# Kernel optimization log

Measured on AMD Instinct MI355X. Metric: run time of the kernel, lower is better.

Reference implementation:

```python
import jax, jax.numpy as jnp
import numpy as np
import math
from jax import lax

B, M, T = 32, 80, 10000
EPS = 1e-6
DELTA_CLAMP = (0.001, 0.1)


def setup_inputs() -> dict:
    key = jax.random.key(0)
    k_mel, = jax.random.split(key, 1)
    # linear mel energies: non-negative
    mel = jax.random.uniform(k_mel, (B, M, T), dtype=jnp.float32)

    def full(v):
        return jnp.full((M,), v, dtype=jnp.float32)

    # exact init values from the torch module
    log_s = full(math.log(0.15 / (1 - 0.15)))
    log_alpha = full(math.log(0.99 / (1 - 0.99)))
    log_delta = full(math.log(0.01))
    log_r = full(math.log(0.1 / (1 - 0.1)))
    return {"mel": mel, "log_s": log_s, "log_alpha": log_alpha,
            "log_delta": log_delta, "log_r": log_r}


def reference(mel, log_s, log_alpha, log_delta, log_r):
    # per-channel coefficients, clamped exactly as in torch
    s = jnp.clip(jax.nn.sigmoid(log_s), 0.05, 0.3)            # (M,)
    alpha = jnp.clip(jax.nn.sigmoid(log_alpha), 0.9, 0.999)   # (M,)
    delta = jnp.clip(jnp.exp(log_delta), *DELTA_CLAMP)        # (M,)
    r = jnp.clip(jax.nn.sigmoid(log_r), 0.05, 0.25)           # (M,)

    # EMA smoother along time via scan. Torch inits smoother = mel[:,:,0]
    # and the t=0 update yields (1-s)*mel0 + s*mel0 = mel0, so we scan over
    # all T frames with init = mel[:,:,0].
    s_bm = s[None, :]                      # (1, M) broadcasts over (B, M)

    def step(smoother, x_t):
        new = (1.0 - s_bm) * smoother + s_bm * x_t
        return new, new

    xs = jnp.moveaxis(mel, -1, 0)          # (T, B, M)
    _, sm = lax.scan(step, mel[:, :, 0], xs)
    smoothed = jnp.moveaxis(sm, 0, -1)     # (B, M, T)

    alpha_c = alpha[None, :, None]
    delta_c = delta[None, :, None]
    r_c = r[None, :, None]

    gain = (EPS + smoothed) ** (-alpha_c)
    pcen = (mel * gain + delta_c) ** r_c - delta_c ** r_c
    return pcen
```

## Files before the change

kernel.cpp:

```cpp
#include <hip/hip_runtime.h>
#include <math.h>


constexpr int B_ = 32, M_ = 80, T_ = 10000;
constexpr int EPI = 256;
constexpr int NFULL = T_ / EPI;
constexpr float EPS_ = 1e-6f;

__device__ __forceinline__ float pcen_one(float x, float y, float alpha,
                                          float delta, float r, float dr) {
    float g = __expf(-alpha * __logf(y + EPS_));
    float z = fmaf(x, g, delta);
    return __expf(r * __logf(z)) - dr;
}

__global__ __launch_bounds__(256) void pcen_kernel(
    const float* __restrict__ mel,
    const float* __restrict__ log_s,
    const float* __restrict__ log_alpha,
    const float* __restrict__ log_delta,
    const float* __restrict__ log_r,
    float* __restrict__ out)
{
    const int lane = threadIdx.x & 63;
    const int wave = threadIdx.x >> 6;
    const int row  = blockIdx.x * 4 + wave;
    if (row >= B_ * M_) return;
    const int m = row % M_;

    float s = 1.0f / (1.0f + __expf(-log_s[m]));
    s = fminf(fmaxf(s, 0.05f), 0.3f);
    float alpha = 1.0f / (1.0f + __expf(-log_alpha[m]));
    alpha = fminf(fmaxf(alpha, 0.9f), 0.999f);
    float delta = __expf(log_delta[m]);
    delta = fminf(fmaxf(delta, 0.001f), 0.1f);
    float r = 1.0f / (1.0f + __expf(-log_r[m]));
    r = fminf(fmaxf(r, 0.05f), 0.25f);

    const float a  = 1.0f - s;
    const float dr = __expf(r * __logf(delta));
    const float a2 = a * a, a3 = a2 * a, a4 = a2 * a2;
    const float c0 = a4, c1 = c0 * c0, c2 = c1 * c1,
                c3 = c2 * c2, c4 = c3 * c3, c5 = c4 * c4;
    const float a256  = c5 * c5;
    const float a4lane = __expf(__logf(a) * (float)(4 * lane));

    const size_t rb = (size_t)row * T_;
    const float* mp = mel + rb;
    float*       op = out + rb;

    float yprev = mp[0];

    float4 x = *(const float4*)(mp + lane * 4);

    for (int it = 0; it < NFULL; ++it) {
        float4 xn = make_float4(0.f, 0.f, 0.f, 0.f);
        if (it + 1 < NFULL)
            xn = *(const float4*)(mp + (size_t)(it + 1) * EPI + lane * 4);

        float l0 = s * x.x;
        float l1 = fmaf(a, l0, s * x.y);
        float l2 = fmaf(a, l1, s * x.z);
        float l3 = fmaf(a, l2, s * x.w);

        float S = l3, t;
        t = __shfl_up(S, 1);  if (lane >= 1)  S = fmaf(c0, t, S);
        t = __shfl_up(S, 2);  if (lane >= 2)  S = fmaf(c1, t, S);
        t = __shfl_up(S, 4);  if (lane >= 4)  S = fmaf(c2, t, S);
        t = __shfl_up(S, 8);  if (lane >= 8)  S = fmaf(c3, t, S);
        t = __shfl_up(S, 16); if (lane >= 16) S = fmaf(c4, t, S);
        t = __shfl_up(S, 32); if (lane >= 32) S = fmaf(c5, t, S);

        float Sp = __shfl_up(S, 1);
        float C  = fmaf(a4lane, yprev, (lane == 0) ? 0.0f : Sp);

        float y0 = fmaf(a,  C, l0);
        float y1 = fmaf(a2, C, l1);
        float y2 = fmaf(a3, C, l2);
        float y3 = fmaf(a4, C, l3);

        float S63 = __shfl(S, 63);
        yprev = fmaf(a256, yprev, S63);

        float4 o;
        o.x = pcen_one(x.x, y0, alpha, delta, r, dr);
        o.y = pcen_one(x.y, y1, alpha, delta, r, dr);
        o.z = pcen_one(x.z, y2, alpha, delta, r, dr);
        o.w = pcen_one(x.w, y3, alpha, delta, r, dr);
        *(float4*)(op + (size_t)it * EPI + lane * 4) = o;

        x = xn;
    }

    {
        const int base = NFULL * EPI + lane * 4;
        const bool act = (base + 3 < T_);
        float4 xt = act ? *(const float4*)(mp + base)
                        : make_float4(0.f, 0.f, 0.f, 0.f);

        float l0 = s * xt.x;
        float l1 = fmaf(a, l0, s * xt.y);
        float l2 = fmaf(a, l1, s * xt.z);
        float l3 = fmaf(a, l2, s * xt.w);

        float S = l3, t;
        t = __shfl_up(S, 1);  if (lane >= 1)  S = fmaf(c0, t, S);
        t = __shfl_up(S, 2);  if (lane >= 2)  S = fmaf(c1, t, S);
        t = __shfl_up(S, 4);  if (lane >= 4)  S = fmaf(c2, t, S);
        t = __shfl_up(S, 8);  if (lane >= 8)  S = fmaf(c3, t, S);
        t = __shfl_up(S, 16); if (lane >= 16) S = fmaf(c4, t, S);
        t = __shfl_up(S, 32); if (lane >= 32) S = fmaf(c5, t, S);

        float Sp = __shfl_up(S, 1);
        float C  = fmaf(a4lane, yprev, (lane == 0) ? 0.0f : Sp);

        if (act) {
            float y0 = fmaf(a,  C, l0);
            float y1 = fmaf(a2, C, l1);
            float y2 = fmaf(a3, C, l2);
            float y3 = fmaf(a4, C, l3);
            float4 o;
            o.x = pcen_one(xt.x, y0, alpha, delta, r, dr);
            o.y = pcen_one(xt.y, y1, alpha, delta, r, dr);
            o.z = pcen_one(xt.z, y2, alpha, delta, r, dr);
            o.w = pcen_one(xt.w, y3, alpha, delta, r, dr);
            *(float4*)(op + base) = o;
        }
    }
}

extern "C" void kernel_launch(void* const* d_in, const int* in_sizes, int n_in,
                              void* d_out, int out_size, void* d_ws, size_t ws_size,
                              hipStream_t stream) {
    const float* mel       = (const float*)d_in[0];
    const float* log_s     = (const float*)d_in[1];
    const float* log_alpha = (const float*)d_in[2];
    const float* log_delta = (const float*)d_in[3];
    const float* log_r     = (const float*)d_in[4];
    float* out = (float*)d_out;

    const int rows = B_ * M_;
    dim3 grid((rows + 3) / 4);
    pcen_kernel<<<grid, 256, 0, stream>>>(mel, log_s, log_alpha, log_delta,
                                          log_r, out);
}
```

Baseline: 204.8 us.

## Split each row's time scan into chunks with warm-up window per wave

Each row's EMA scan along time is split into 2048-sample chunks, one wave per chunk, which raises the wave count fivefold to fill the GPU and hide latency in the serial scan. A chunk starts its recurrence by re-scanning the 256 samples before it, seeded with a single sample, and relies on the decay (1-s)^256 being negligible instead of carrying the exact state. This adds some redundant reads and compute and introduces a tiny truncation error, which is bounded by the clamp on s. The scan step is moved into a helper function.

```diff
diff --git a/kernel.cpp b/kernel.cpp
--- a/kernel.cpp
+++ b/kernel.cpp
@@ -3,8 +3,10 @@
 
 
 constexpr int B_ = 32, M_ = 80, T_ = 10000;
-constexpr int EPI = 256;
-constexpr int NFULL = T_ / EPI;
+constexpr int EPI   = 256;
+constexpr int CHUNK = 2048;
+constexpr int NCH   = (T_ + CHUNK - 1) / CHUNK;
+constexpr int ITERS = CHUNK / EPI;
 constexpr float EPS_ = 1e-6f;
 
 __device__ __forceinline__ float pcen_one(float x, float y, float alpha,
@@ -12,6 +14,41 @@
     float g = __expf(-alpha * __logf(y + EPS_));
     float z = fmaf(x, g, delta);
     return __expf(r * __logf(z)) - dr;
+}
+
+struct ScanCoef {
+    float s, a, a2, a3, a4;
+    float c0, c1, c2, c3, c4, c5;
+    float a4lane;
+};
+
+__device__ __forceinline__ float scan256(float4 x, const ScanCoef& k, int lane,
+                                         float yprev,
+                                         float& y0, float& y1, float& y2, float& y3) {
+    float l0 = k.s * x.x;
+    float l1 = fmaf(k.a, l0, k.s * x.y);
+    float l2 = fmaf(k.a, l1, k.s * x.z);
+    float l3 = fmaf(k.a, l2, k.s * x.w);
+
+    float S = l3, t;
+    t = __shfl_up(S, 1);  if (lane >= 1)  S = fmaf(k.c0, t, S);
+    t = __shfl_up(S, 2);  if (lane >= 2)  S = fmaf(k.c1, t, S);
+    t = __shfl_up(S, 4);  if (lane >= 4)  S = fmaf(k.c2, t, S);
+    t = __shfl_up(S, 8);  if (lane >= 8)  S = fmaf(k.c3, t, S);
+    t = __shfl_up(S, 16); if (lane >= 16) S = fmaf(k.c4, t, S);
+    t = __shfl_up(S, 32); if (lane >= 32) S = fmaf(k.c5, t, S);
+
+    float Sp = __shfl_up(S, 1);
+    float C  = fmaf(k.a4lane, yprev, (lane == 0) ? 0.0f : Sp);
+
+    y0 = fmaf(k.a,  C, l0);
+    y1 = fmaf(k.a2, C, l1);
+    y2 = fmaf(k.a3, C, l2);
+    y3 = fmaf(k.a4, C, l3);
+
+    float S63 = __shfl(S, 63);
+    float a256 = k.c5 * k.c5;
+    return fmaf(a256, yprev, S63);
 }
 
 __global__ __launch_bounds__(256) void pcen_kernel(
@@ -23,10 +60,12 @@
     float* __restrict__ out)
 {
     const int lane = threadIdx.x & 63;
-    const int wave = threadIdx.x >> 6;
-    const int row  = blockIdx.x * 4 + wave;
-    if (row >= B_ * M_) return;
-    const int m = row % M_;
+    const int wv   = threadIdx.x >> 6;
+    const int gw   = blockIdx.x * 4 + wv;
+    if (gw >= B_ * M_ * NCH) return;
+    const int row = gw / NCH;
+    const int c   = gw % NCH;
+    const int m   = row % M_;
 
     float s = 1.0f / (1.0f + __expf(-log_s[m]));
     s = fminf(fmaxf(s, 0.05f), 0.3f);
@@ -36,96 +75,55 @@
     delta = fminf(fmaxf(delta, 0.001f), 0.1f);
     float r = 1.0f / (1.0f + __expf(-log_r[m]));
     r = fminf(fmaxf(r, 0.05f), 0.25f);
+    const float dr = __expf(r * __logf(delta));
 
-    const float a  = 1.0f - s;
-    const float dr = __expf(r * __logf(delta));
-    const float a2 = a * a, a3 = a2 * a, a4 = a2 * a2;
-    const float c0 = a4, c1 = c0 * c0, c2 = c1 * c1,
-                c3 = c2 * c2, c4 = c3 * c3, c5 = c4 * c4;
-    const float a256  = c5 * c5;
-    const float a4lane = __expf(__logf(a) * (float)(4 * lane));
+    ScanCoef k;
+    k.s = s; k.a = 1.0f - s;
+    k.a2 = k.a * k.a; k.a3 = k.a2 * k.a; k.a4 = k.a2 * k.a2;
+    k.c0 = k.a4; k.c1 = k.c0 * k.c0; k.c2 = k.c1 * k.c1;
+    k.c3 = k.c2 * k.c2; k.c4 = k.c3 * k.c3; k.c5 = k.c4 * k.c4;
+    k.a4lane = __expf(__logf(k.a) * (float)(4 * lane));
 
-    const size_t rb = (size_t)row * T_;
-    const float* mp = mel + rb;
-    float*       op = out + rb;
+    const size_t rb   = (size_t)row * T_;
+    const float* mp   = mel + rb;
+    float*       op   = out + rb;
+    const int    start = c * CHUNK;
 
-    float yprev = mp[0];
+    float yprev;
+    float y0, y1, y2, y3;
 
-    float4 x = *(const float4*)(mp + lane * 4);
-
-    for (int it = 0; it < NFULL; ++it) {
-        float4 xn = make_float4(0.f, 0.f, 0.f, 0.f);
-        if (it + 1 < NFULL)
-            xn = *(const float4*)(mp + (size_t)(it + 1) * EPI + lane * 4);
-
-        float l0 = s * x.x;
-        float l1 = fmaf(a, l0, s * x.y);
-        float l2 = fmaf(a, l1, s * x.z);
-        float l3 = fmaf(a, l2, s * x.w);
-
-        float S = l3, t;
-        t = __shfl_up(S, 1);  if (lane >= 1)  S = fmaf(c0, t, S);
-        t = __shfl_up(S, 2);  if (lane >= 2)  S = fmaf(c1, t, S);
-        t = __shfl_up(S, 4);  if (lane >= 4)  S = fmaf(c2, t, S);
-        t = __shfl_up(S, 8);  if (lane >= 8)  S = fmaf(c3, t, S);
-        t = __shfl_up(S, 16); if (lane >= 16) S = fmaf(c4, t, S);
-        t = __shfl_up(S, 32); if (lane >= 32) S = fmaf(c5, t, S);
-
-        float Sp = __shfl_up(S, 1);
-        float C  = fmaf(a4lane, yprev, (lane == 0) ? 0.0f : Sp);
-
-        float y0 = fmaf(a,  C, l0);
-        float y1 = fmaf(a2, C, l1);
-        float y2 = fmaf(a3, C, l2);
-        float y3 = fmaf(a4, C, l3);
-
-        float S63 = __shfl(S, 63);
-        yprev = fmaf(a256, yprev, S63);
-
-        float4 o;
-        o.x = pcen_one(x.x, y0, alpha, delta, r, dr);
-        o.y = pcen_one(x.y, y1, alpha, delta, r, dr);
-        o.z = pcen_one(x.z, y2, alpha, delta, r, dr);
-        o.w = pcen_one(x.w, y3, alpha, delta, r, dr);
-        *(float4*)(op + (size_t)it * EPI + lane * 4) = o;
-
-        x = xn;
+    if (c == 0) {
+        float4 xh = *(const float4*)(mp + lane * 4);
+        yprev = __shfl(xh.x, 0);
+    } else {
+        float4 xh = *(const float4*)(mp + (start - EPI) + lane * 4);
+        yprev = __shfl(xh.x, 0);
+        yprev = scan256(xh, k, lane, yprev, y0, y1, y2, y3);
     }
 
-    {
-        const int base = NFULL * EPI + lane * 4;
-        const bool act = (base + 3 < T_);
-        float4 xt = act ? *(const float4*)(mp + base)
-                        : make_float4(0.f, 0.f, 0.f, 0.f);
+    int base = start + lane * 4;
+    bool act = base < T_;
+    float4 x = act ? *(const float4*)(mp + base)
+                   : make_float4(0.f, 0.f, 0.f, 0.f);
 
-        float l0 = s * xt.x;
-        float l1 = fmaf(a, l0, s * xt.y);
-        float l2 = fmaf(a, l1, s * xt.z);
-        float l3 = fmaf(a, l2, s * xt.w);
+    for (int it = 0; it < ITERS; ++it) {
+        int   base_n = base + EPI;
+        bool  act_n  = (it + 1 < ITERS) && (base_n < T_);
+        float4 xn = act_n ? *(const float4*)(mp + base_n)
+                          : make_float4(0.f, 0.f, 0.f, 0.f);
 
-        float S = l3, t;
-        t = __shfl_up(S, 1);  if (lane >= 1)  S = fmaf(c0, t, S);
-        t = __shfl_up(S, 2);  if (lane >= 2)  S = fmaf(c1, t, S);
-        t = __shfl_up(S, 4);  if (lane >= 4)  S = fmaf(c2, t, S);
-        t = __shfl_up(S, 8);  if (lane >= 8)  S = fmaf(c3, t, S);
-        t = __shfl_up(S, 16); if (lane >= 16) S = fmaf(c4, t, S);
-        t = __shfl_up(S, 32); if (lane >= 32) S = fmaf(c5, t, S);
-
-        float Sp = __shfl_up(S, 1);
-        float C  = fmaf(a4lane, yprev, (lane == 0) ? 0.0f : Sp);
+        yprev = scan256(x, k, lane, yprev, y0, y1, y2, y3);
 
         if (act) {
-            float y0 = fmaf(a,  C, l0);
-            float y1 = fmaf(a2, C, l1);
-            float y2 = fmaf(a3, C, l2);
-            float y3 = fmaf(a4, C, l3);
             float4 o;
-            o.x = pcen_one(xt.x, y0, alpha, delta, r, dr);
-            o.y = pcen_one(xt.y, y1, alpha, delta, r, dr);
-            o.z = pcen_one(xt.z, y2, alpha, delta, r, dr);
-            o.w = pcen_one(xt.w, y3, alpha, delta, r, dr);
+            o.x = pcen_one(x.x, y0, alpha, delta, r, dr);
+            o.y = pcen_one(x.y, y1, alpha, delta, r, dr);
+            o.z = pcen_one(x.z, y2, alpha, delta, r, dr);
+            o.w = pcen_one(x.w, y3, alpha, delta, r, dr);
             *(float4*)(op + base) = o;
         }
+
+        x = xn; base = base_n; act = act_n;
     }
 }
 
@@ -139,8 +137,8 @@
     const float* log_r     = (const float*)d_in[4];
     float* out = (float*)d_out;
 
-    const int rows = B_ * M_;
-    dim3 grid((rows + 3) / 4);
+    const int nwaves = B_ * M_ * NCH;
+    dim3 grid((nwaves + 3) / 4);
     pcen_kernel<<<grid, 256, 0, stream>>>(mel, log_s, log_alpha, log_delta,
                                           log_r, out);
 }
```

After: 196.6 us. 1.04x faster.
